# Optimization experiments

Hardware: AMD Instinct MI355X
Metric: run time of the kernel (lower is better)

The kernel has to match this reference:

```python
import jax, jax.numpy as jnp
import numpy as np

DIM = 1024
N_HEADS = 16
HD = DIM // N_HEADS


def setup_inputs() -> dict:
    key = jax.random.key(0)
    k1, k2, k3 = jax.random.split(key, 3)
    x = jax.random.normal(k1, (4, 2048, DIM), dtype=jnp.float32)
    # torch nn.Linear weights: W_qkv [3*dim, dim], W_proj [dim, dim]; y = x @ W.T
    W_qkv = jax.random.normal(k2, (3 * DIM, DIM), dtype=jnp.float32) * 0.02
    W_proj = jax.random.normal(k3, (DIM, DIM), dtype=jnp.float32) * 0.02
    return {"x": x, "W_qkv": W_qkv, "W_proj": W_proj}


def reference(x, W_qkv, W_proj):
    B, T, D = x.shape
    H, hd = N_HEADS, HD
    # fused QKV projection: (B,T,3D)
    qkv = jnp.einsum('btd,ed->bte', x, W_qkv)
    # view(B,T,3,H,hd).transpose(1,2) -> (B,3,T,H,hd)
    qkv = qkv.reshape(B, T, 3, H, hd).transpose(0, 2, 1, 3, 4)
    q, k, v = qkv[:, 0], qkv[:, 1], qkv[:, 2]  # each (B,T,H,hd)
    # NOTE: faithful to source — SDPA sees (B,T) as batch dims and attends
    # over the heads axis (length H), NOT the sequence axis.
    scale = 1.0 / np.sqrt(hd).astype(np.float32)
    scores = jnp.einsum('btie,btje->btij', q, k) * scale  # (B,T,H,H)
    attn = jax.nn.softmax(scores, axis=-1)
    out = jnp.einsum('btij,btje->btie', attn, v)  # (B,T,H,hd)
    # out.transpose(1,2).contiguous().view(B,T,D)
    out = out.transpose(0, 2, 1, 3).reshape(B, T, D)
    return jnp.einsum('btd,ed->bte', out, W_proj)
```

## Files before the change

kernel.cpp:

```cpp
#include <hip/hip_runtime.h>


typedef __bf16 bf16x8 __attribute__((ext_vector_type(8)));
typedef float  f32x4  __attribute__((ext_vector_type(4)));

typedef __attribute__((address_space(3))) void       lds_void;
typedef const __attribute__((address_space(1))) void gbl_void;

__device__ __forceinline__ float b2f(unsigned short u) {
    union { unsigned int i; float f; } c; c.i = ((unsigned int)u) << 16; return c.f;
}
__device__ __forceinline__ unsigned short f2b(float f) {
    unsigned int u = __builtin_bit_cast(unsigned int, f);
    return (unsigned short)((u + 0x7FFFu + ((u >> 16) & 1u)) >> 16);
}
__device__ __forceinline__ unsigned int pack2(float a, float b) {
    return (unsigned int)f2b(a) | ((unsigned int)f2b(b) << 16);
}
__device__ __forceinline__ void unpack8(uint4 u, float* f) {
    unsigned int w[4] = {u.x, u.y, u.z, u.w};
#pragma unroll
    for (int a = 0; a < 4; ++a) {
        union { unsigned int i; float f; } lo, hi;
        lo.i = w[a] << 16;
        hi.i = w[a] & 0xFFFF0000u;
        f[a * 2]     = lo.f;
        f[a * 2 + 1] = hi.f;
    }
}

__global__ __launch_bounds__(256) void cvt_f32_bf16(const float* __restrict__ in,
                                                    unsigned short* __restrict__ out,
                                                    int n4) {
    int i = blockIdx.x * 256 + threadIdx.x;
    if (i >= n4) return;
    float4 f = reinterpret_cast<const float4*>(in)[i];
    ushort4 u;
    u.x = f2b(f.x); u.y = f2b(f.y); u.z = f2b(f.z); u.w = f2b(f.w);
    reinterpret_cast<ushort4*>(out)[i] = u;
}

__device__ __forceinline__ void store_c(float* C, long idx, float v)          { C[idx] = v; }
__device__ __forceinline__ void store_c(unsigned short* C, long idx, float v) { C[idx] = f2b(v); }

template <typename CT>
__global__ __launch_bounds__(256) void gemm_bt(const unsigned short* __restrict__ A,
                                               const unsigned short* __restrict__ B,
                                               CT* __restrict__ C,
                                               int M, int N, int K) {
    __shared__ __align__(16) unsigned short As[128 * 64];
    __shared__ __align__(16) unsigned short Bs[128 * 64];

    const int tid  = threadIdx.x;
    const int lane = tid & 63;
    const int wave = tid >> 6;
    const long bm  = blockIdx.y;
    const long bn  = blockIdx.x;
    const int wm   = (wave >> 1) * 64;
    const int wn   = (wave & 1) * 64;

    f32x4 acc[4][4] = {};

    const unsigned short* Ab = A + bm * 128 * (long)K;
    const unsigned short* Bb = B + bn * 128 * (long)K;

    const int srow = tid >> 3;
    const int scol = (tid & 7) * 8;

    for (int k0 = 0; k0 < K; k0 += 64) {
#pragma unroll
        for (int r = 0; r < 4; ++r) {
            const int row = r * 32 + srow;
            __builtin_amdgcn_global_load_lds(
                (gbl_void*)(Ab + (long)row * K + k0 + scol),
                (lds_void*)(As + (r * 256 + wave * 64) * 8), 16, 0, 0);
        }
#pragma unroll
        for (int r = 0; r < 4; ++r) {
            const int row = r * 32 + srow;
            __builtin_amdgcn_global_load_lds(
                (gbl_void*)(Bb + (long)row * K + k0 + scol),
                (lds_void*)(Bs + (r * 256 + wave * 64) * 8), 16, 0, 0);
        }
        __syncthreads();

#pragma unroll
        for (int kk = 0; kk < 64; kk += 32) {
            const int lcol = kk + ((lane >> 4) << 3);
            bf16x8 af[4], bfr[4];
#pragma unroll
            for (int i = 0; i < 4; ++i) {
                af[i]  = *reinterpret_cast<const bf16x8*>(As + (wm + i * 16 + (lane & 15)) * 64 + lcol);
                bfr[i] = *reinterpret_cast<const bf16x8*>(Bs + (wn + i * 16 + (lane & 15)) * 64 + lcol);
            }
#pragma unroll
            for (int i = 0; i < 4; ++i)
#pragma unroll
                for (int j = 0; j < 4; ++j)
                    acc[i][j] = __builtin_amdgcn_mfma_f32_16x16x32_bf16(af[i], bfr[j], acc[i][j], 0, 0, 0);
        }
        __syncthreads();
    }

    const long mrow0 = bm * 128 + wm + ((lane >> 4) << 2);
    const long ncol0 = bn * 128 + wn + (lane & 15);
#pragma unroll
    for (int i = 0; i < 4; ++i)
#pragma unroll
        for (int j = 0; j < 4; ++j)
#pragma unroll
            for (int r = 0; r < 4; ++r)
                store_c(C, (mrow0 + i * 16 + r) * (long)N + ncol0 + j * 16, acc[i][j][r]);
}

__global__ __launch_bounds__(256) void attn_rowlocal(const unsigned short* __restrict__ qkv,
                                                     unsigned short* __restrict__ out3) {
    __shared__ __align__(16) unsigned short rows[4][3072];
    __shared__ float attnS[4][16][16];

    const int tid  = threadIdx.x;
    const int lane = tid & 63;
    const int wave = tid >> 6;
    const int m0   = blockIdx.x * 4;

    {
        const uint4* src = reinterpret_cast<const uint4*>(qkv + (long)m0 * 3072);
        uint4* dst = reinterpret_cast<uint4*>(&rows[0][0]);
#pragma unroll
        for (int c = 0; c < 6; ++c) dst[c * 256 + tid] = src[c * 256 + tid];
    }
    __syncthreads();

    const int m = m0 + wave;
    const int b = m >> 11;
    const int t = m & 2047;
    const unsigned short* q = rows[wave];
    const unsigned short* k = q + 1024;
    const unsigned short* v = q + 2048;

    const int i  = lane & 15;
    const int j0 = (lane >> 4) << 2;
    float sc[4] = {0.f, 0.f, 0.f, 0.f};
#pragma unroll
    for (int dc = 0; dc < 64; dc += 8) {
        uint4 qu = *reinterpret_cast<const uint4*>(q + i * 64 + dc);
        float qf[8];
        unpack8(qu, qf);
#pragma unroll
        for (int jj = 0; jj < 4; ++jj) {
            uint4 ku = *reinterpret_cast<const uint4*>(k + (j0 + jj) * 64 + dc);
            float kf[8];
            unpack8(ku, kf);
#pragma unroll
            for (int d = 0; d < 8; ++d) sc[jj] += qf[d] * kf[d];
        }
    }
#pragma unroll
    for (int jj = 0; jj < 4; ++jj) sc[jj] *= 0.125f;

    float mx = fmaxf(fmaxf(sc[0], sc[1]), fmaxf(sc[2], sc[3]));
    mx = fmaxf(mx, __shfl_xor(mx, 16));
    mx = fmaxf(mx, __shfl_xor(mx, 32));
    float sum = 0.f;
#pragma unroll
    for (int jj = 0; jj < 4; ++jj) { sc[jj] = __expf(sc[jj] - mx); sum += sc[jj]; }
    sum += __shfl_xor(sum, 16);
    sum += __shfl_xor(sum, 32);
    const float inv = 1.0f / sum;
#pragma unroll
    for (int jj = 0; jj < 4; ++jj) attnS[wave][i][j0 + jj] = sc[jj] * inv;
    __syncthreads();

    const int oi = lane >> 2;
    const int s0 = (lane & 3) << 4;
    float o[16];
#pragma unroll
    for (int s = 0; s < 16; ++s) o[s] = 0.f;
#pragma unroll
    for (int j = 0; j < 16; ++j) {
        const float a = attnS[wave][oi][j];
        const unsigned short* vp = v + j * 64 + s0;
        uint4 v0 = *reinterpret_cast<const uint4*>(vp);
        uint4 v1 = *reinterpret_cast<const uint4*>(vp + 8);
        float vf[16];
        unpack8(v0, vf);
        unpack8(v1, vf + 8);
#pragma unroll
        for (int s = 0; s < 16; ++s) o[s] += a * vf[s];
    }

    uint4 r0, r1;
    r0.x = pack2(o[0],  o[1]);  r0.y = pack2(o[2],  o[3]);
    r0.z = pack2(o[4],  o[5]);  r0.w = pack2(o[6],  o[7]);
    r1.x = pack2(o[8],  o[9]);  r1.y = pack2(o[10], o[11]);
    r1.z = pack2(o[12], o[13]); r1.w = pack2(o[14], o[15]);

    const long base = (long)b * (2048 * 1024)
                    + (long)(oi * 128 + (t >> 4)) * 1024
                    + 64 * (t & 15) + s0;
    *reinterpret_cast<uint4*>(out3 + base)     = r0;
    *reinterpret_cast<uint4*>(out3 + base + 8) = r1;
}

extern "C" void kernel_launch(void* const* d_in, const int* in_sizes, int n_in,
                              void* d_out, int out_size, void* d_ws, size_t ws_size,
                              hipStream_t stream) {
    const float* x     = (const float*)d_in[0];
    const float* Wqkv  = (const float*)d_in[1];
    const float* Wproj = (const float*)d_in[2];
    float* out = (float*)d_out;

    char* ws = (char*)d_ws;
    unsigned short* xb     = (unsigned short*)(ws);
    unsigned short* wqkvb  = (unsigned short*)(ws + 16777216);
    unsigned short* wprojb = (unsigned short*)(ws + 23068672);
    unsigned short* qkvb   = (unsigned short*)(ws + 25165824);
    unsigned short* out3b  = (unsigned short*)(ws + 75497472);

    cvt_f32_bf16<<<dim3(8192), dim3(256), 0, stream>>>(x,     xb,     2097152);
    cvt_f32_bf16<<<dim3(3072), dim3(256), 0, stream>>>(Wqkv,  wqkvb,   786432);
    cvt_f32_bf16<<<dim3(1024), dim3(256), 0, stream>>>(Wproj, wprojb,  262144);

    gemm_bt<unsigned short><<<dim3(24, 64), dim3(256), 0, stream>>>(
        xb, wqkvb, qkvb, 8192, 3072, 1024);

    attn_rowlocal<<<dim3(2048), dim3(256), 0, stream>>>(qkvb, out3b);

    gemm_bt<float><<<dim3(8, 64), dim3(256), 0, stream>>>(
        out3b, wprojb, out, 8192, 1024, 1024);
}
```

Baseline: 225.8 us.

## Switch GEMM to 32x32 MFMA with XOR-swizzled LDS and smaller proj tiles

```diff
diff --git a/kernel.cpp b/kernel.cpp
--- a/kernel.cpp
+++ b/kernel.cpp
@@ -2,14 +2,11 @@
 
 
 typedef __bf16 bf16x8 __attribute__((ext_vector_type(8)));
-typedef float  f32x4  __attribute__((ext_vector_type(4)));
+typedef float  f32x16 __attribute__((ext_vector_type(16)));
 
 typedef __attribute__((address_space(3))) void       lds_void;
 typedef const __attribute__((address_space(1))) void gbl_void;
 
-__device__ __forceinline__ float b2f(unsigned short u) {
-    union { unsigned int i; float f; } c; c.i = ((unsigned int)u) << 16; return c.f;
-}
 __device__ __forceinline__ unsigned short f2b(float f) {
     unsigned int u = __builtin_bit_cast(unsigned int, f);
     return (unsigned short)((u + 0x7FFFu + ((u >> 16) & 1u)) >> 16);
@@ -43,13 +40,14 @@
 __device__ __forceinline__ void store_c(float* C, long idx, float v)          { C[idx] = v; }
 __device__ __forceinline__ void store_c(unsigned short* C, long idx, float v) { C[idx] = f2b(v); }
 
-template <typename CT>
+template <int BN, typename CT>
 __global__ __launch_bounds__(256) void gemm_bt(const unsigned short* __restrict__ A,
                                                const unsigned short* __restrict__ B,
                                                CT* __restrict__ C,
                                                int M, int N, int K) {
+    constexpr int NT = BN / 64;
     __shared__ __align__(16) unsigned short As[128 * 64];
-    __shared__ __align__(16) unsigned short Bs[128 * 64];
+    __shared__ __align__(16) unsigned short Bs[BN * 64];
 
     const int tid  = threadIdx.x;
     const int lane = tid & 63;
@@ -57,66 +55,68 @@
     const long bm  = blockIdx.y;
     const long bn  = blockIdx.x;
     const int wm   = (wave >> 1) * 64;
-    const int wn   = (wave & 1) * 64;
-
-    f32x4 acc[4][4] = {};
+    const int wn   = (wave & 1) * (BN / 2);
+
+    f32x16 acc[2][NT] = {};
 
     const unsigned short* Ab = A + bm * 128 * (long)K;
-    const unsigned short* Bb = B + bn * 128 * (long)K;
-
-    const int srow = tid >> 3;
-    const int scol = (tid & 7) * 8;
+    const unsigned short* Bb = B + bn * BN * (long)K;
+
+    const int srow  = tid >> 3;
+    const int sgcol = ((tid & 7) ^ (srow & 7)) << 3;
 
     for (int k0 = 0; k0 < K; k0 += 64) {
 #pragma unroll
-        for (int r = 0; r < 4; ++r) {
-            const int row = r * 32 + srow;
+        for (int r = 0; r < 4; ++r)
             __builtin_amdgcn_global_load_lds(
-                (gbl_void*)(Ab + (long)row * K + k0 + scol),
+                (gbl_void*)(Ab + (long)(r * 32 + srow) * K + k0 + sgcol),
                 (lds_void*)(As + (r * 256 + wave * 64) * 8), 16, 0, 0);
-        }
-#pragma unroll
-        for (int r = 0; r < 4; ++r) {
-            const int row = r * 32 + srow;
+#pragma unroll
+        for (int r = 0; r < BN / 32; ++r)
             __builtin_amdgcn_global_load_lds(
-                (gbl_void*)(Bb + (long)row * K + k0 + scol),
+                (gbl_void*)(Bb + (long)(r * 32 + srow) * K + k0 + sgcol),
                 (lds_void*)(Bs + (r * 256 + wave * 64) * 8), 16, 0, 0);
+        __syncthreads();
+
+        const int arow = lane & 31;
+        const int kh   = lane >> 5;
+#pragma unroll
+        for (int kk = 0; kk < 4; ++kk) {
+            const int c  = kk * 2 + kh;
+            const int sw = (c ^ (lane & 7)) << 3;
+            bf16x8 af[2], bfr[NT];
+#pragma unroll
+            for (int i = 0; i < 2; ++i)
+                af[i] = *reinterpret_cast<const bf16x8*>(As + (wm + i * 32 + arow) * 64 + sw);
+#pragma unroll
+            for (int j = 0; j < NT; ++j)
+                bfr[j] = *reinterpret_cast<const bf16x8*>(Bs + (wn + j * 32 + arow) * 64 + sw);
+#pragma unroll
+            for (int i = 0; i < 2; ++i)
+#pragma unroll
+                for (int j = 0; j < NT; ++j)
+                    acc[i][j] = __builtin_amdgcn_mfma_f32_32x32x16_bf16(af[i], bfr[j], acc[i][j], 0, 0, 0);
         }
         __syncthreads();
-
-#pragma unroll
-        for (int kk = 0; kk < 64; kk += 32) {
-            const int lcol = kk + ((lane >> 4) << 3);
-            bf16x8 af[4], bfr[4];
-#pragma unroll
-            for (int i = 0; i < 4; ++i) {
-                af[i]  = *reinterpret_cast<const bf16x8*>(As + (wm + i * 16 + (lane & 15)) * 64 + lcol);
-                bfr[i] = *reinterpret_cast<const bf16x8*>(Bs + (wn + i * 16 + (lane & 15)) * 64 + lcol);
+    }
+
+    const long mbase = bm * 128 + wm + ((lane >> 5) << 2);
+    const long nbase = bn * BN + wn + (lane & 31);
+#pragma unroll
+    for (int i = 0; i < 2; ++i)
+#pragma unroll
+        for (int j = 0; j < NT; ++j)
+#pragma unroll
+            for (int r = 0; r < 16; ++r) {
+                const long row = mbase + i * 32 + (r & 3) + 8 * (r >> 2);
+                store_c(C, row * (long)N + nbase + j * 32, acc[i][j][r]);
             }
-#pragma unroll
-            for (int i = 0; i < 4; ++i)
-#pragma unroll
-                for (int j = 0; j < 4; ++j)
-                    acc[i][j] = __builtin_amdgcn_mfma_f32_16x16x32_bf16(af[i], bfr[j], acc[i][j], 0, 0, 0);
-        }
-        __syncthreads();
-    }
-
-    const long mrow0 = bm * 128 + wm + ((lane >> 4) << 2);
-    const long ncol0 = bn * 128 + wn + (lane & 15);
-#pragma unroll
-    for (int i = 0; i < 4; ++i)
-#pragma unroll
-        for (int j = 0; j < 4; ++j)
-#pragma unroll
-            for (int r = 0; r < 4; ++r)
-                store_c(C, (mrow0 + i * 16 + r) * (long)N + ncol0 + j * 16, acc[i][j][r]);
 }
 
 __global__ __launch_bounds__(256) void attn_rowlocal(const unsigned short* __restrict__ qkv,
                                                      unsigned short* __restrict__ out3) {
-    __shared__ __align__(16) unsigned short rows[4][3072];
-    __shared__ float attnS[4][16][16];
+    __shared__ __align__(16) unsigned short rows[4 * 3072];
+    __shared__ float attnS[4][16][17];
 
     const int tid  = threadIdx.x;
     const int lane = tid & 63;
@@ -125,30 +125,33 @@
 
     {
         const uint4* src = reinterpret_cast<const uint4*>(qkv + (long)m0 * 3072);
-        uint4* dst = reinterpret_cast<uint4*>(&rows[0][0]);
-#pragma unroll
-        for (int c = 0; c < 6; ++c) dst[c * 256 + tid] = src[c * 256 + tid];
+        uint4* dst = reinterpret_cast<uint4*>(rows);
+#pragma unroll
+        for (int c = 0; c < 6; ++c) {
+            const int S  = c * 256 + tid;
+            const int gs = (S & ~7) | ((S & 7) ^ ((S >> 3) & 7));
+            dst[S] = src[gs];
+        }
     }
     __syncthreads();
 
     const int m = m0 + wave;
     const int b = m >> 11;
     const int t = m & 2047;
-    const unsigned short* q = rows[wave];
-    const unsigned short* k = q + 1024;
-    const unsigned short* v = q + 2048;
+    const unsigned short* rw = rows + wave * 3072;
 
     const int i  = lane & 15;
     const int j0 = (lane >> 4) << 2;
     float sc[4] = {0.f, 0.f, 0.f, 0.f};
 #pragma unroll
-    for (int dc = 0; dc < 64; dc += 8) {
-        uint4 qu = *reinterpret_cast<const uint4*>(q + i * 64 + dc);
+    for (int c8 = 0; c8 < 8; ++c8) {
+        uint4 qu = *reinterpret_cast<const uint4*>(rw + i * 64 + ((c8 ^ (i & 7)) << 3));
         float qf[8];
         unpack8(qu, qf);
 #pragma unroll
         for (int jj = 0; jj < 4; ++jj) {
-            uint4 ku = *reinterpret_cast<const uint4*>(k + (j0 + jj) * 64 + dc);
+            const int vi = 16 + j0 + jj;
+            uint4 ku = *reinterpret_cast<const uint4*>(rw + vi * 64 + ((c8 ^ (vi & 7)) << 3));
             float kf[8];
             unpack8(ku, kf);
 #pragma unroll
@@ -173,15 +176,16 @@
 
     const int oi = lane >> 2;
     const int s0 = (lane & 3) << 4;
+    const int c0 = (lane & 3) << 1;
     float o[16];
 #pragma unroll
     for (int s = 0; s < 16; ++s) o[s] = 0.f;
 #pragma unroll
     for (int j = 0; j < 16; ++j) {
-        const float a = attnS[wave][oi][j];
-        const unsigned short* vp = v + j * 64 + s0;
-        uint4 v0 = *reinterpret_cast<const uint4*>(vp);
-        uint4 v1 = *reinterpret_cast<const uint4*>(vp + 8);
+        const float a  = attnS[wave][oi][j];
+        const int   vi = 32 + j;
+        uint4 v0 = *reinterpret_cast<const uint4*>(rw + vi * 64 + (((c0)     ^ (vi & 7)) << 3));
+        uint4 v1 = *reinterpret_cast<const uint4*>(rw + vi * 64 + (((c0 + 1) ^ (vi & 7)) << 3));
         float vf[16];
         unpack8(v0, vf);
         unpack8(v1, vf + 8);
@@ -221,11 +225,11 @@
     cvt_f32_bf16<<<dim3(3072), dim3(256), 0, stream>>>(Wqkv,  wqkvb,   786432);
     cvt_f32_bf16<<<dim3(1024), dim3(256), 0, stream>>>(Wproj, wprojb,  262144);
 
-    gemm_bt<unsigned short><<<dim3(24, 64), dim3(256), 0, stream>>>(
+    gemm_bt<128, unsigned short><<<dim3(24, 64), dim3(256), 0, stream>>>(
         xb, wqkvb, qkvb, 8192, 3072, 1024);
 
     attn_rowlocal<<<dim3(2048), dim3(256), 0, stream>>>(qkvb, out3b);
 
-    gemm_bt<float><<<dim3(8, 64), dim3(256), 0, stream>>>(
+    gemm_bt<64, float><<<dim3(16, 64), dim3(256), 0, stream>>>(
         out3b, wprojb, out, 8192, 1024, 1024);
 }
```

Result: faster. 206.8 us (-8.4%).
